# Performance work log

Measured on AMD Instinct MI355X. Metric: run time of the kernel, lower is better.

Reference implementation:

```python
import jax, jax.numpy as jnp
import numpy as np
import math

B, Q, K, D = 16, 2048, 2048, 128


def setup_inputs() -> dict:
    key = jax.random.key(0)
    kq, kk, kv, kl = jax.random.split(key, 4)
    queries = jax.random.normal(kq, (B, Q, D), dtype=jnp.float32)
    keys = jax.random.normal(kk, (B, K, D), dtype=jnp.float32)
    values = jax.random.normal(kv, (B, K, D), dtype=jnp.float32)
    valid_lens = jax.random.randint(kl, (B,), 1, K + 1, dtype=jnp.int32)
    return {"queries": queries, "keys": keys, "values": values, "valid_lens": valid_lens}


def reference(queries, keys, values, valid_lens):
    d = queries.shape[-1]
    # scores = bmm(Q, K^T) // sqrt(d)  -- source uses floor-division, kept faithfully
    scores = jnp.floor(jnp.einsum('bqd,bkd->bqk', queries, keys) / math.sqrt(d))
    # masked_softmax: positions >= valid_len[b] get -1e6 before softmax
    mask = jnp.arange(keys.shape[1]) < valid_lens[:, None, None]  # [B,1,K]
    scores = jnp.where(mask, scores, -1e6)
    attn = jax.nn.softmax(scores, axis=-1)
    # dropout in eval mode = identity
    return jnp.einsum('bqk,bkv->bqv', attn, values)
```

## Files before the change

### kernel.cpp

```cpp
#include <hip/hip_runtime.h>
#include <cmath>

typedef __attribute__((ext_vector_type(4))) float f32x4;
typedef __attribute__((ext_vector_type(8))) _Float16 f16x8;
typedef __attribute__((ext_vector_type(4))) _Float16 f16x4;
typedef __attribute__((ext_vector_type(4))) unsigned int u32x4;

#define B_SZ 16
#define Q_SZ 2048
#define K_SZ 2048
#define D_SZ 128
#define BQ   64
#define BKT  64
#define SCL  0.08838834764831845f

#define GLDS16(g, s) __builtin_amdgcn_global_load_lds(                      \
    (const __attribute__((address_space(1))) unsigned int*)(g),             \
    (__attribute__((address_space(3))) unsigned int*)(s), 16, 0, 0)

static __device__ inline unsigned pk16(float a, float b) {
  unsigned short ha = __builtin_bit_cast(unsigned short, (_Float16)a);
  unsigned short hb = __builtin_bit_cast(unsigned short, (_Float16)b);
  return (unsigned)ha | ((unsigned)hb << 16);
}

__global__ __launch_bounds__(256) void prep_all(
    const float* __restrict__ K, const float* __restrict__ V,
    _Float16* __restrict__ Khi, _Float16* __restrict__ Klo,
    _Float16* __restrict__ Vt, unsigned* __restrict__ cnt)
{
  __shared__ _Float16 tmp[64][136];
  const int tid = threadIdx.x;
  if (cnt && blockIdx.x == 0 && tid == 0) *cnt = 0;
  if (blockIdx.x < 2048) {
    const int gid = blockIdx.x * 256 + tid;
    const int r = gid >> 4;
    const int g = gid & 15;
    const float* src = K + (size_t)r * D_SZ + g * 8;
    f16x8 hi, lo;
#pragma unroll
    for (int i = 0; i < 8; ++i) {
      float x = src[i];
      _Float16 h = (_Float16)x;
      hi[i] = h;
      lo[i] = (_Float16)((x - (float)h) * 2048.0f);
    }
    const size_t o = (size_t)r * D_SZ + ((g ^ (r & 7)) * 8);
    *(f16x8*)(Khi + o) = hi;
    *(f16x8*)(Klo + o) = lo;
  } else {
    const int vb = blockIdx.x - 2048;
    const int b = vb >> 5;
    const int k0 = (vb & 31) * 64;
    const float* Vb = V + ((size_t)b * K_SZ + k0) * D_SZ;
#pragma unroll
    for (int j = 0; j < 8; ++j) {
      const int e = j * 1024 + tid * 4;
      const int k = e >> 7, d = e & 127;
      const f32x4 v = *(const f32x4*)(Vb + (size_t)k * D_SZ + d);
      f16x4 h;
#pragma unroll
      for (int i = 0; i < 4; ++i) h[i] = (_Float16)v[i];
      *(f16x4*)&tmp[k][d] = h;
    }
    __syncthreads();
#pragma unroll
    for (int i = 0; i < 4; ++i) {
      const int id = i * 256 + tid;
      const int gk = id >> 7, d = id & 127;
      f16x8 o;
#pragma unroll
      for (int jj = 0; jj < 8; ++jj) {
        const int kap = ((gk >> 2) << 5) | ((jj >> 2) << 4) | ((gk & 3) << 2) | (jj & 3);
        o[jj] = tmp[kap][d];
      }
      _Float16* dst = Vt + ((size_t)b * D_SZ + d) * K_SZ + k0 + ((gk ^ (d & 7)) * 8);
      *(f16x8*)dst = o;
    }
  }
}

__global__ __launch_bounds__(256, 3) void attn(
    const float* __restrict__ Qm, const _Float16* __restrict__ KhiG,
    const _Float16* __restrict__ KloG, const _Float16* __restrict__ VtG,
    const int* __restrict__ vlp, float* __restrict__ Om,
    float* __restrict__ P1, float* __restrict__ L0, float* __restrict__ L1,
    unsigned* __restrict__ cnt, const int split)
{
  __shared__ __align__(16) char sm[49152];
  __shared__ float Ls[64];
  __shared__ int s_task;
  __shared__ signed char ord[32];
  __shared__ int vls[16];

  const int tid  = threadIdx.x;
  const int wave = tid >> 6;
  const int lane = tid & 63;
  const int ln   = lane & 15;
  const int quad = lane >> 4;

  _Float16* smKhi = (_Float16*)sm;
  _Float16* smKlo = (_Float16*)(sm + 16384);
  _Float16* smVt  = (_Float16*)(sm + 32768);

  if (split) {
    if (tid < 16) vls[tid] = vlp[tid];
    __syncthreads();
    if (tid < 32) {
      const int ub = tid >> 1, uh = tid & 1;
      const int v = vls[ub];
      const int n = uh ? ((v > 1024) ? (v - 1024 + 63) / 64 : 0)
                       : (((v < 1024 ? v : 1024) + 63) / 64);
      int rank = 0;
      for (int u = 0; u < 32; ++u) {
        const int wb = u >> 1, wh = u & 1;
        const int wv = vls[wb];
        const int wn = wh ? ((wv > 1024) ? (wv - 1024 + 63) / 64 : 0)
                          : (((wv < 1024 ? wv : 1024) + 63) / 64);
        rank += (wn > n) || (wn == n && u < tid);
      }
      ord[rank] = (signed char)tid;
    }
    __syncthreads();
  }

  for (;;) {
    int t;
    if (split) {
      if (tid == 0) s_task = (int)atomicAdd(cnt, 1u);
      __syncthreads();
      t = s_task;
      __syncthreads();
      if (t >= 1024) return;
    } else {
      t = blockIdx.x;
    }

    int half = 0, b, qt;
    if (split) { const int u = ord[t >> 5]; b = u >> 1; half = u & 1; qt = t & 31; }
    else       { b = t >> 5; qt = t & 31; }
    const int q0     = qt * BQ;
    const int valid  = split ? vls[b] : vlp[b];
    const int kstart = half * 1024;
    const int kend   = split ? min(valid, kstart + 1024) : valid;
    if (kend <= kstart) { if (!split) return; continue; }
    const int ntiles = (kend - kstart + BKT - 1) / BKT;

    const float* Qb    = Qm + (size_t)b * Q_SZ * D_SZ;
    const char*  gKhiB = (const char*)KhiG + (size_t)b * K_SZ * 256;
    const char*  gKloB = (const char*)KloG + (size_t)b * K_SZ * 256;
    const char*  gVtB  = (const char*)VtG  + (size_t)b * D_SZ * (K_SZ * 2);

    f16x8 qhi[4], qlo[4];
    {
      const int qrow = q0 + wave * 16 + ln;
      const float* srcb = Qb + (size_t)qrow * D_SZ + quad * 8;
#pragma unroll
      for (int c = 0; c < 4; ++c) {
#pragma unroll
        for (int j = 0; j < 8; ++j) {
          float x = srcb[c * 32 + j];
          _Float16 h = (_Float16)x;
          qhi[c][j] = h;
          qlo[c][j] = (_Float16)((x - (float)h) * 2048.0f);
        }
      }
    }

    const f32x4 vzero = {0.f, 0.f, 0.f, 0.f};
    f32x4 accO[8];
    float lsum = 0.0f;
#pragma unroll
    for (int dt = 0; dt < 8; ++dt) accO[dt] = vzero;

    for (int kt = 0; kt < ntiles; ++kt) {
      const int k0g = kstart + kt * BKT;

      if (kt) {
        asm volatile("s_waitcnt lgkmcnt(0)" ::: "memory");
        __builtin_amdgcn_sched_barrier(0);
        __builtin_amdgcn_s_barrier();
        __builtin_amdgcn_sched_barrier(0);
      }

      {
        const char* gh = gKhiB + (size_t)k0g * 256;
        const char* gl = gKloB + (size_t)k0g * 256;
#pragma unroll
        for (int i = 0; i < 4; ++i) {
          const int off = wave * 1024 + i * 4096;
          GLDS16(gh + off + lane * 16, sm + off);
        }
#pragma unroll
        for (int i = 0; i < 4; ++i) {
          const int off = wave * 1024 + i * 4096;
          GLDS16(gl + off + lane * 16, sm + 16384 + off);
        }
#pragma unroll
        for (int i = 0; i < 4; ++i) {
          const int off = wave * 1024 + i * 4096;
          const int a = off + lane * 16;
          const int d = a >> 7, win = a & 127;
          GLDS16(gVtB + (size_t)d * (K_SZ * 2) + (size_t)k0g * 2 + win,
                 sm + 32768 + off);
        }
      }
      asm volatile("s_waitcnt vmcnt(0)" ::: "memory");
      __builtin_amdgcn_sched_barrier(0);
      __builtin_amdgcn_s_barrier();
      __builtin_amdgcn_sched_barrier(0);

      f16x8 pa[2];
#pragma unroll
      for (int hk = 0; hk < 2; ++hk) {
        f32x4 accM[2], accC[2];
#pragma unroll
        for (int nb2 = 0; nb2 < 2; ++nb2) { accM[nb2] = vzero; accC[nb2] = vzero; }
        __builtin_amdgcn_s_setprio(1);
#pragma unroll
        for (int nb2 = 0; nb2 < 2; ++nb2) {
          const int row = (hk * 2 + nb2) * 16 + ln;
          const _Float16* bh_base = smKhi + row * 128;
          const _Float16* bl_base = smKlo + row * 128;
#pragma unroll
          for (int c = 0; c < 4; ++c) {
            const int pg = (((c * 4 + quad) ^ (ln & 7)) * 8);
            const f16x8 bh = *(const f16x8*)(bh_base + pg);
            const f16x8 bl = *(const f16x8*)(bl_base + pg);
            accM[nb2] = __builtin_amdgcn_mfma_f32_16x16x32_f16(bh, qhi[c], accM[nb2], 0, 0, 0);
            accC[nb2] = __builtin_amdgcn_mfma_f32_16x16x32_f16(bl, qhi[c], accC[nb2], 0, 0, 0);
            accC[nb2] = __builtin_amdgcn_mfma_f32_16x16x32_f16(bh, qlo[c], accC[nb2], 0, 0, 0);
          }
        }
        __builtin_amdgcn_s_setprio(0);

        u32x4 w;
#pragma unroll
        for (int nb2 = 0; nb2 < 2; ++nb2) {
          float e[4];
#pragma unroll
          for (int r = 0; r < 4; ++r) {
            const int key = k0g + (hk * 2 + nb2) * 16 + quad * 4 + r;
            const float s = accM[nb2][r] + accC[nb2][r] * (1.0f / 2048.0f);
            e[r] = (key < valid) ? __expf(floorf(s * SCL)) : 0.0f;
            lsum += e[r];
          }
          w[nb2 * 2 + 0] = pk16(e[0], e[1]);
          w[nb2 * 2 + 1] = pk16(e[2], e[3]);
        }
        pa[hk] = __builtin_bit_cast(f16x8, w);
      }

      __builtin_amdgcn_s_setprio(1);
#pragma unroll
      for (int c = 0; c < 2; ++c) {
#pragma unroll
        for (int dt = 0; dt < 8; ++dt) {
          const int drow = dt * 16 + ln;
          const int pg = (((c * 4 + quad) ^ (ln & 7)) * 8);
          const f16x8 bf = *(const f16x8*)(smVt + drow * 64 + pg);
          accO[dt] = __builtin_amdgcn_mfma_f32_16x16x32_f16(pa[c], bf, accO[dt], 0, 0, 0);
        }
      }
      __builtin_amdgcn_s_setprio(0);
    }

    {
      float v = lsum;
      v += __shfl_xor(v, 16, 64);
      v += __shfl_xor(v, 32, 64);
      lsum = v;
    }

    if (split) {
      float* Lh = half ? L1 : L0;
      if (lane < 16)
        Lh[b * Q_SZ + q0 + wave * 16 + lane] = lsum;
      float* dst = (half ? P1 : Om) + ((size_t)(b * Q_SZ + q0)) * D_SZ;
#pragma unroll
      for (int dt = 0; dt < 8; ++dt)
#pragma unroll
        for (int r = 0; r < 4; ++r)
          dst[(size_t)(wave * 16 + quad * 4 + r) * D_SZ + dt * 16 + ln] =
              accO[dt][r];
    } else {
      if (lane < 16) Ls[wave * 16 + lane] = lsum;
      __syncthreads();
      float* Ob = Om + (size_t)b * Q_SZ * D_SZ;
#pragma unroll
      for (int r = 0; r < 4; ++r) {
        const float inv = 1.0f / Ls[wave * 16 + quad * 4 + r];
#pragma unroll
        for (int dt = 0; dt < 8; ++dt)
          Ob[(size_t)(q0 + wave * 16 + quad * 4 + r) * D_SZ + dt * 16 + ln] =
              accO[dt][r] * inv;
      }
    }
    if (!split) return;
  }
}

__global__ __launch_bounds__(256) void finalize(
    float* __restrict__ Om, const float* __restrict__ P1,
    const float* __restrict__ L0, const float* __restrict__ L1,
    const int* __restrict__ vlp)
{
  const int idx = blockIdx.x * 256 + threadIdx.x;
  const size_t e = (size_t)idx * 4;
  const int row = (int)(e >> 7);
  const int b = row >> 11;
  const int valid = vlp[b];
  f32x4 o = *(const f32x4*)(Om + e);
  float l = L0[row];
  if (valid > 1024) {
    const f32x4 p = *(const f32x4*)(P1 + e);
    o += p;
    l += L1[row];
  }
  const float inv = 1.0f / l;
  o *= inv;
  *(f32x4*)(Om + e) = o;
}

extern "C" void kernel_launch(void* const* d_in, const int* in_sizes, int n_in,
                              void* d_out, int out_size, void* d_ws, size_t ws_size,
                              hipStream_t stream) {
  const float* Qm = (const float*)d_in[0];
  const float* Km = (const float*)d_in[1];
  const float* Vm = (const float*)d_in[2];
  const int*   vl = (const int*)d_in[3];
  float*       Om = (float*)d_out;

  const size_t elems = (size_t)B_SZ * K_SZ * D_SZ;
  const size_t PREP  = 3 * elems * sizeof(_Float16);
  const size_t HDR   = 262400;
  const size_t P1SZ  = elems * sizeof(float);
  char* W = (char*)d_ws;

  if (ws_size >= HDR + PREP + P1SZ) {
    unsigned* cnt = (unsigned*)W;
    float*    L0  = (float*)(W + 256);
    float*    L1  = (float*)(W + 256 + 131072);
    _Float16* Khi = (_Float16*)(W + HDR);
    _Float16* Klo = Khi + elems;
    _Float16* Vt  = Klo + elems;
    float*    P1  = (float*)(W + HDR + PREP);
    prep_all<<<2560, 256, 0, stream>>>(Km, Vm, Khi, Klo, Vt, cnt);
    attn<<<768, 256, 0, stream>>>(Qm, Khi, Klo, Vt, vl, Om, P1, L0, L1, cnt, 1);
    finalize<<<4096, 256, 0, stream>>>(Om, P1, L0, L1, vl);
  } else {
    _Float16* Khi = (_Float16*)W;
    _Float16* Klo = Khi + elems;
    _Float16* Vt  = Klo + elems;
    prep_all<<<2560, 256, 0, stream>>>(Km, Vm, Khi, Klo, Vt, nullptr);
    attn<<<512, 256, 0, stream>>>(Qm, Khi, Klo, Vt, vl, Om,
                                  nullptr, nullptr, nullptr, nullptr, 0);
  }
}
```

Before: 160.6 us.

## Double-buffer K/V tiles with 32-key tiles and async prefetch

Halves the key tile size to 32 and splits LDS into two 24 KB buffers, so the next tile's global-to-LDS loads are issued before computing on the current tile and waited on with a partial vmcnt. The V-transpose swizzle in the prep kernel and in the PV reads changes to match the 32-key row layout. This is meant to hide global load latency behind MFMA work. In exchange each tile now takes two barriers and does less work, so synchronisation overhead per key rises.

```diff
diff --git a/kernel.cpp b/kernel.cpp
--- a/kernel.cpp
+++ b/kernel.cpp
@@ -11,7 +11,8 @@
 #define K_SZ 2048
 #define D_SZ 128
 #define BQ   64
-#define BKT  64
+#define BKT  32
+#define BUF  24576
 #define SCL  0.08838834764831845f
 
 #define GLDS16(g, s) __builtin_amdgcn_global_load_lds(                      \
@@ -68,13 +69,15 @@
     for (int i = 0; i < 4; ++i) {
       const int id = i * 256 + tid;
       const int gk = id >> 7, d = id & 127;
+      const int s = gk >> 2, g2 = gk & 3;
       f16x8 o;
 #pragma unroll
       for (int jj = 0; jj < 8; ++jj) {
-        const int kap = ((gk >> 2) << 5) | ((jj >> 2) << 4) | ((gk & 3) << 2) | (jj & 3);
+        const int kap = (s << 5) | ((jj >> 2) << 4) | (g2 << 2) | (jj & 3);
         o[jj] = tmp[kap][d];
       }
-      _Float16* dst = Vt + ((size_t)b * D_SZ + d) * K_SZ + k0 + ((gk ^ (d & 7)) * 8);
+      const int cs = (g2 ^ (d & 3) ^ ((d >> 2) & 3)) & 3;
+      _Float16* dst = Vt + ((size_t)b * D_SZ + d) * K_SZ + k0 + s * 32 + cs * 8;
       *(f16x8*)dst = o;
     }
   }
@@ -87,7 +90,7 @@
     float* __restrict__ P1, float* __restrict__ L0, float* __restrict__ L1,
     unsigned* __restrict__ cnt, const int split)
 {
-  __shared__ __align__(16) char sm[49152];
+  __shared__ __align__(16) char sm[2 * BUF];
   __shared__ float Ls[64];
   __shared__ int s_task;
   __shared__ signed char ord[32];
@@ -98,10 +101,6 @@
   const int lane = tid & 63;
   const int ln   = lane & 15;
   const int quad = lane >> 4;
-
-  _Float16* smKhi = (_Float16*)sm;
-  _Float16* smKlo = (_Float16*)(sm + 16384);
-  _Float16* smVt  = (_Float16*)(sm + 32768);
 
   if (split) {
     if (tid < 16) vls[tid] = vlp[tid];
@@ -151,6 +150,29 @@
     const char*  gKloB = (const char*)KloG + (size_t)b * K_SZ * 256;
     const char*  gVtB  = (const char*)VtG  + (size_t)b * D_SZ * (K_SZ * 2);
 
+    auto STAGE = [&](int k0g, char* buf) {
+      const char* gh = gKhiB + (size_t)k0g * 256;
+      const char* gl = gKloB + (size_t)k0g * 256;
+#pragma unroll
+      for (int i = 0; i < 2; ++i) {
+        const int off = wave * 1024 + i * 4096;
+        GLDS16(gh + off + lane * 16, buf + off);
+      }
+#pragma unroll
+      for (int i = 0; i < 2; ++i) {
+        const int off = wave * 1024 + i * 4096;
+        GLDS16(gl + off + lane * 16, buf + 8192 + off);
+      }
+#pragma unroll
+      for (int i = 0; i < 2; ++i) {
+        const int off = wave * 1024 + i * 4096;
+        const int a = off + lane * 16;
+        const int d = a >> 6, win = a & 63;
+        GLDS16(gVtB + (size_t)d * (K_SZ * 2) + (size_t)k0g * 2 + win,
+               buf + 16384 + off);
+      }
+    };
+
     f16x8 qhi[4], qlo[4];
     {
       const int qrow = q0 + wave * 16 + ln;
@@ -173,53 +195,34 @@
 #pragma unroll
     for (int dt = 0; dt < 8; ++dt) accO[dt] = vzero;
 
+    STAGE(kstart, sm);
+
     for (int kt = 0; kt < ntiles; ++kt) {
+      char* cbuf = sm + (kt & 1) * BUF;
+      _Float16* smKhi = (_Float16*)cbuf;
+      _Float16* smKlo = (_Float16*)(cbuf + 8192);
+      _Float16* smVt  = (_Float16*)(cbuf + 16384);
       const int k0g = kstart + kt * BKT;
 
-      if (kt) {
-        asm volatile("s_waitcnt lgkmcnt(0)" ::: "memory");
-        __builtin_amdgcn_sched_barrier(0);
-        __builtin_amdgcn_s_barrier();
-        __builtin_amdgcn_sched_barrier(0);
-      }
-
-      {
-        const char* gh = gKhiB + (size_t)k0g * 256;
-        const char* gl = gKloB + (size_t)k0g * 256;
-#pragma unroll
-        for (int i = 0; i < 4; ++i) {
-          const int off = wave * 1024 + i * 4096;
-          GLDS16(gh + off + lane * 16, sm + off);
-        }
-#pragma unroll
-        for (int i = 0; i < 4; ++i) {
-          const int off = wave * 1024 + i * 4096;
-          GLDS16(gl + off + lane * 16, sm + 16384 + off);
-        }
-#pragma unroll
-        for (int i = 0; i < 4; ++i) {
-          const int off = wave * 1024 + i * 4096;
-          const int a = off + lane * 16;
-          const int d = a >> 7, win = a & 127;
-          GLDS16(gVtB + (size_t)d * (K_SZ * 2) + (size_t)k0g * 2 + win,
-                 sm + 32768 + off);
-        }
-      }
-      asm volatile("s_waitcnt vmcnt(0)" ::: "memory");
+      if (kt + 1 < ntiles) {
+        STAGE(kstart + (kt + 1) * BKT, sm + ((kt + 1) & 1) * BUF);
+        asm volatile("s_waitcnt vmcnt(6)" ::: "memory");
+      } else {
+        asm volatile("s_waitcnt vmcnt(0)" ::: "memory");
+      }
       __builtin_amdgcn_sched_barrier(0);
       __builtin_amdgcn_s_barrier();
       __builtin_amdgcn_sched_barrier(0);
 
-      f16x8 pa[2];
-#pragma unroll
-      for (int hk = 0; hk < 2; ++hk) {
+      f16x8 pa;
+      {
         f32x4 accM[2], accC[2];
 #pragma unroll
         for (int nb2 = 0; nb2 < 2; ++nb2) { accM[nb2] = vzero; accC[nb2] = vzero; }
         __builtin_amdgcn_s_setprio(1);
 #pragma unroll
         for (int nb2 = 0; nb2 < 2; ++nb2) {
-          const int row = (hk * 2 + nb2) * 16 + ln;
+          const int row = nb2 * 16 + ln;
           const _Float16* bh_base = smKhi + row * 128;
           const _Float16* bl_base = smKlo + row * 128;
 #pragma unroll
@@ -240,7 +243,7 @@
           float e[4];
 #pragma unroll
           for (int r = 0; r < 4; ++r) {
-            const int key = k0g + (hk * 2 + nb2) * 16 + quad * 4 + r;
+            const int key = k0g + nb2 * 16 + quad * 4 + r;
             const float s = accM[nb2][r] + accC[nb2][r] * (1.0f / 2048.0f);
             e[r] = (key < valid) ? __expf(floorf(s * SCL)) : 0.0f;
             lsum += e[r];
@@ -248,21 +251,22 @@
           w[nb2 * 2 + 0] = pk16(e[0], e[1]);
           w[nb2 * 2 + 1] = pk16(e[2], e[3]);
         }
-        pa[hk] = __builtin_bit_cast(f16x8, w);
+        pa = __builtin_bit_cast(f16x8, w);
       }
 
       __builtin_amdgcn_s_setprio(1);
 #pragma unroll
-      for (int c = 0; c < 2; ++c) {
-#pragma unroll
-        for (int dt = 0; dt < 8; ++dt) {
-          const int drow = dt * 16 + ln;
-          const int pg = (((c * 4 + quad) ^ (ln & 7)) * 8);
-          const f16x8 bf = *(const f16x8*)(smVt + drow * 64 + pg);
-          accO[dt] = __builtin_amdgcn_mfma_f32_16x16x32_f16(pa[c], bf, accO[dt], 0, 0, 0);
-        }
+      for (int dt = 0; dt < 8; ++dt) {
+        const int drow = dt * 16 + ln;
+        const int pg = ((quad ^ (drow & 3) ^ ((drow >> 2) & 3)) & 3) * 8;
+        const f16x8 bf = *(const f16x8*)(smVt + drow * 32 + pg);
+        accO[dt] = __builtin_amdgcn_mfma_f32_16x16x32_f16(pa, bf, accO[dt], 0, 0, 0);
       }
       __builtin_amdgcn_s_setprio(0);
+
+      __builtin_amdgcn_sched_barrier(0);
+      __builtin_amdgcn_s_barrier();
+      __builtin_amdgcn_sched_barrier(0);
     }
 
     {
```

Result: slower. 164.2 us (+2.3%).
